# Kernel optimization log

Hardware: AMD Instinct MI355X
Metric: run time of the kernel (lower is better)

## Reference

```python
import jax, jax.numpy as jnp
import numpy as np

B, S, E, H = 4, 2048, 1024, 16
D = E // H


def setup_inputs() -> dict:
    key = jax.random.key(0)
    ks = jax.random.split(key, 6)
    scale = 1.0 / np.sqrt(E).astype(np.float32)
    return {
        "x": jax.random.normal(ks[0], (B, S, E), jnp.float32),
        # positive entries -> cumsum normalizer is well conditioned
        "weight": jax.random.uniform(ks[1], (H, S), jnp.float32, 0.05, 1.0),
        "bias": jax.random.normal(ks[2], (H, S), jnp.float32) * 0.02,
        "inp_w": jax.random.normal(ks[3], (E, E), jnp.float32) * scale,
        "inp_b": jax.random.normal(ks[4], (E,), jnp.float32) * 0.02,
        "out_w": jax.random.normal(ks[5], (E, E), jnp.float32) * scale,
    }


def reference(x, weight, bias, inp_w, inp_b, out_w):
    Bx, Sx, Ex = x.shape
    Hx = weight.shape[0]
    Dx = Ex // Hx
    # input projection (torch Linear: x @ W.T + b)
    x = x @ inp_w.T + inp_b
    # (B,S,E) -> (B,E,S) -> (B,H,D,S)
    xh = x.transpose(0, 2, 1).reshape(Bx, Hx, Dx, Sx)
    # Toeplitz causal matrix per head: M[h,i,j] = weight[h, j-i] if j>=i else 0
    idx = jnp.arange(Sx)
    off = idx[None, :] - idx[:, None]  # (S,S)
    M = jnp.where(off >= 0, weight[:, off], jnp.zeros((), x.dtype))  # (H,S,S)
    # batched matmul over the sequence axis: y[b,h,d,t] = sum_s x[b,h,d,s] M[h,s,t]
    y = jnp.einsum('bhds,hst->bhdt', xh, M)
    # cumulative-sum normalization (do_toep_mean=True)
    norm = jnp.cumsum(weight, axis=-1)  # (H,S)
    y = y / norm[None, :, None, :]
    # per-head, per-position bias
    y = y + bias[None, :, None, :]
    # (B,H,D,S) -> (B,E,S) -> (B,S,E)
    y = y.reshape(Bx, Ex, Sx).transpose(0, 2, 1)
    # output projection (no bias)
    return y @ out_w.T
```

## Files before the change

kernel.cpp:

```cpp
#include <hip/hip_runtime.h>

typedef unsigned short u16;
typedef __attribute__((ext_vector_type(4))) float f32x4;
typedef __attribute__((ext_vector_type(8))) __bf16 bf16x8;

__device__ __forceinline__ u16 f2bf(float f) {
  unsigned u = __builtin_bit_cast(unsigned, f);
  u = u + 0x7fffu + ((u >> 16) & 1u);
  return (u16)(u >> 16);
}

__device__ __forceinline__ void load_lds16(const void* g, void* l) {
  __builtin_amdgcn_global_load_lds((__attribute__((address_space(1))) void*)g,
                                   (__attribute__((address_space(3))) void*)l,
                                   16, 0, 0);
}

__device__ __forceinline__ f32x4 MF(bf16x8 a, bf16x8 b, f32x4 c) {
  return __builtin_amdgcn_mfma_f32_16x16x32_bf16(a, b, c, 0, 0, 0);
}

__global__ __launch_bounds__(256) void prep_all(const float* __restrict__ x,
                                                const float* __restrict__ inp_w,
                                                const float* __restrict__ out_w,
                                                const float* __restrict__ weight,
                                                u16* __restrict__ Xb,
                                                u16* __restrict__ Wb,
                                                u16* __restrict__ OWb,
                                                float* __restrict__ normB,
                                                u16* __restrict__ V) {
  const int bx = blockIdx.x, tid = threadIdx.x;
  if (bx < 10240) {
    const float* src; u16* dst; int i;
    if (bx < 8192)      { src = x;     dst = Xb;  i = bx * 256 + tid; }
    else if (bx < 9216) { src = inp_w; dst = Wb;  i = (bx - 8192) * 256 + tid; }
    else                { src = out_w; dst = OWb; i = (bx - 9216) * 256 + tid; }
    const float4 v = ((const float4*)src)[i];
    ushort4 o;
    o.x = f2bf(v.x); o.y = f2bf(v.y); o.z = f2bf(v.z); o.w = f2bf(v.w);
    ((ushort4*)dst)[i] = o;
    return;
  }
  if (bx < 10256) {
    const int h = bx - 10240;
    __shared__ float ts[256];
    float v[8];
    const float* src = weight + h * 2048 + tid * 8;
    float s = 0.f;
#pragma unroll
    for (int j = 0; j < 8; ++j) v[j] = src[j];
#pragma unroll
    for (int j = 0; j < 8; ++j) { s += v[j]; v[j] = s; }
    ts[tid] = s;
    __syncthreads();
    float xx = s;
#pragma unroll
    for (int d = 1; d < 256; d <<= 1) {
      float y = (tid >= d) ? ts[tid - d] : 0.f;
      __syncthreads();
      xx += y;
      ts[tid] = xx;
      __syncthreads();
    }
    const float excl = xx - s;
    float* dst = normB + h * 2048 + tid * 8;
#pragma unroll
    for (int j = 0; j < 8; ++j) dst[j] = excl + v[j];
    return;
  }
  {
    const int bb = bx - 10256;
    const int h = bb & 15, tb = bb >> 4;
    __shared__ u16 wl[2048];
#pragma unroll
    for (int j = 0; j < 8; ++j) wl[tid * 8 + j] = f2bf(weight[h * 2048 + tid * 8 + j]);
    __syncthreads();
#pragma unroll
    for (int i = 0; i < 8; ++i) {
      const int cid = i * 256 + tid;
      const int row = cid >> 4, c = cid & 15;
      const int t = tb * 128 + row;
      const int j0 = c * 8;
      unsigned v[8];
#pragma unroll
      for (int jj = 0; jj < 8; ++jj) {
        const int j = j0 + jj;
        v[jj] = (t >= j) ? (unsigned)wl[t - j] : 0u;
      }
      uint4 o;
      o.x = v[0] | (v[1] << 16); o.y = v[2] | (v[3] << 16);
      o.z = v[4] | (v[5] << 16); o.w = v[6] | (v[7] << 16);
      *(uint4*)(V + ((size_t)(h * 2048 + t)) * 128 + j0) = o;
    }
  }
}

template <bool BIAS, bool F32OUT, int DEC>
__global__ __launch_bounds__(256) void gemm_nt4(const u16* __restrict__ A,
                                                const u16* __restrict__ B,
                                                void* __restrict__ C,
                                                const float* __restrict__ bias,
                                                int K, int lda, int ldb, int ldc) {
  __shared__ __align__(16) u16 As[2][128 * 64];
  __shared__ __align__(16) u16 Bs[2][128 * 64];
  const int tid = threadIdx.x;
  const int lane = tid & 63, wv = tid >> 6;
  const int wm = wv >> 1, wn = wv & 1;
  const int l15 = lane & 15, g = lane >> 4;

  const int flat = (int)blockIdx.x;
  int m0, n0;
  if (DEC == 0) {
    const int xcd = flat & 7, i = flat >> 3;
    m0 = (i & 7) * 128;
    n0 = ((xcd << 3) + (i >> 3)) * 128;
  } else {
    const int sw = (flat & 7) * 64 + (flat >> 3);
    m0 = (sw >> 3) * 128;
    n0 = (sw & 7) * 128;
  }

  const int NT = K >> 6;

  auto stage = [&](int t, int bi) {
    const int kt = t << 6;
#pragma unroll
    for (int i = 0; i < 4; ++i) {
      const int c = i * 256 + tid;
      const int row = c >> 3, cc = c & 7;
      load_lds16(A + (size_t)(m0 + row) * lda + kt + ((cc ^ (row & 7)) << 3),
                 &As[bi][i * 2048 + wv * 512]);
    }
#pragma unroll
    for (int i = 0; i < 4; ++i) {
      const int c = i * 256 + tid;
      const int row = c >> 3, cc = c & 7;
      load_lds16(B + (size_t)(n0 + row) * ldb + kt + ((cc ^ (row & 7)) << 3),
                 &Bs[bi][i * 2048 + wv * 512]);
    }
  };

  f32x4 acc[4][4] = {};
  stage(0, 0);
  __syncthreads();
  int cur = 0;
  for (int t = 0; t < NT; ++t) {
    if (t + 1 < NT) stage(t + 1, cur ^ 1);
#pragma unroll
    for (int kh = 0; kh < 2; ++kh) {
      bf16x8 af[4], bf[4];
#pragma unroll
      for (int mf = 0; mf < 4; ++mf) {
        const int row = wm * 64 + mf * 16 + l15;
        af[mf] = *(const bf16x8*)(&As[cur][row * 64 + ((((kh << 2) + g) ^ (row & 7)) << 3)]);
      }
#pragma unroll
      for (int nf = 0; nf < 4; ++nf) {
        const int row = wn * 64 + nf * 16 + l15;
        bf[nf] = *(const bf16x8*)(&Bs[cur][row * 64 + ((((kh << 2) + g) ^ (row & 7)) << 3)]);
      }
      __builtin_amdgcn_s_setprio(1);
#pragma unroll
      for (int mf = 0; mf < 4; ++mf)
#pragma unroll
        for (int nf = 0; nf < 4; ++nf)
          acc[mf][nf] = MF(af[mf], bf[nf], acc[mf][nf]);
      __builtin_amdgcn_s_setprio(0);
    }
    __syncthreads();
    cur ^= 1;
  }

#pragma unroll
  for (int mf = 0; mf < 4; ++mf) {
#pragma unroll
    for (int r = 0; r < 4; ++r) {
      const int row = m0 + wm * 64 + mf * 16 + g * 4 + r;
      const float bb = BIAS ? bias[row] : 0.f;
#pragma unroll
      for (int nf = 0; nf < 4; ++nf) {
        const int col = n0 + wn * 64 + nf * 16 + l15;
        const float v = acc[mf][nf][r] + bb;
        if (F32OUT)
          ((float*)C)[(size_t)row * ldc + col] = v;
        else
          ((u16*)C)[(size_t)row * ldc + col] = f2bf(v);
      }
    }
  }
}

__global__ __launch_bounds__(256) void toep_conv(const u16* __restrict__ X1t,
                                                 const u16* __restrict__ V,
                                                 const float* __restrict__ normB,
                                                 const float* __restrict__ biasB,
                                                 u16* __restrict__ Y2b) {
  __shared__ __align__(16) u16 As[3][128 * 64];
  __shared__ __align__(16) u16 Xs[3][64 * 64];
  const int tid = threadIdx.x;
  const int lane = tid & 63, wv = tid >> 6;
  const int l15 = lane & 15, g = lane >> 4;

  const int x = (int)blockIdx.x;
  const int h = (x & 7) + 8 * ((x >> 3) & 1);
  const int pb = x >> 4;
  const int pair = pb & 7, b = pb >> 3;

  const u16* Vh = V + (size_t)h * 2048 * 128;
  const u16* Xrow = X1t + (size_t)h * 64 * 8192 + b * 2048;

#pragma unroll 1
  for (int ti = 0; ti < 2; ++ti) {
    const int tt = ti ? pair : 15 - pair;
    const int t0 = tt * 128;
    const int Q = (tt + 1) * 2;
    f32x4 acc[2][4] = {};

    auto stage = [&](int q, int bufi) {
      const int st = q >> 1, k = q & 1;
      const int s0 = st * 128 + k * 64;
#pragma unroll
      for (int i = 0; i < 2; ++i) {
        const int c = i * 256 + tid;
        const int row = c >> 3, cc = c & 7;
        load_lds16(Xrow + (size_t)row * 8192 + s0 + ((cc ^ (row & 7)) * 8),
                   &Xs[bufi][i * 2048 + wv * 512]);
      }
      const u16* Ab = Vh + (size_t)(tt - st) * 128 * 128 + k * 64;
#pragma unroll
      for (int i = 0; i < 4; ++i) {
        const int c = i * 256 + tid;
        const int row = c >> 3, cc = c & 7;
        load_lds16(Ab + row * 128 + ((cc ^ (row & 7)) * 8),
                   &As[bufi][i * 2048 + wv * 512]);
      }
    };

    stage(0, 0);
    if (Q > 1) stage(1, 1);
    asm volatile("s_waitcnt vmcnt(6)" ::: "memory");
    __builtin_amdgcn_sched_barrier(0);
    __builtin_amdgcn_s_barrier();
    asm volatile("" ::: "memory");

    int cur = 0;
    for (int q = 0; q < Q; ++q) {
      if (q + 2 < Q) stage(q + 2, (q + 2) % 3);
#pragma unroll
      for (int ks = 0; ks < 2; ++ks) {
        bf16x8 af[2];
#pragma unroll
        for (int tf = 0; tf < 2; ++tf) {
          const int row = wv * 32 + tf * 16 + l15;
          af[tf] = *(const bf16x8*)(&As[cur][row * 64 + (((ks * 4 + g) ^ (row & 7)) * 8)]);
        }
        __builtin_amdgcn_s_setprio(1);
#pragma unroll
        for (int nf = 0; nf < 4; ++nf) {
          const int row = nf * 16 + l15;
          const bf16x8 bv = *(const bf16x8*)(&Xs[cur][row * 64 + (((ks * 4 + g) ^ (row & 7)) * 8)]);
#pragma unroll
          for (int tf = 0; tf < 2; ++tf)
            acc[tf][nf] = MF(af[tf], bv, acc[tf][nf]);
        }
        __builtin_amdgcn_s_setprio(0);
      }
      if (q + 2 < Q)      asm volatile("s_waitcnt vmcnt(6)" ::: "memory");
      else if (q + 1 < Q) asm volatile("s_waitcnt vmcnt(0)" ::: "memory");
      __builtin_amdgcn_sched_barrier(0);
      __builtin_amdgcn_s_barrier();
      asm volatile("" ::: "memory");
      cur = (cur == 2) ? 0 : cur + 1;
    }

#pragma unroll
    for (int tf = 0; tf < 2; ++tf) {
#pragma unroll
      for (int r = 0; r < 4; ++r) {
        const int t = t0 + wv * 32 + tf * 16 + g * 4 + r;
        const float inv = 1.0f / normB[h * 2048 + t];
        const float bb = biasB[h * 2048 + t];
#pragma unroll
        for (int nf = 0; nf < 4; ++nf) {
          const int d = nf * 16 + l15;
          Y2b[(size_t)(b * 2048 + t) * 1024 + h * 64 + d] = f2bf(acc[tf][nf][r] * inv + bb);
        }
      }
    }
  }
}

extern "C" void kernel_launch(void* const* d_in, const int* in_sizes, int n_in,
                              void* d_out, int out_size, void* d_ws, size_t ws_size,
                              hipStream_t stream) {
  (void)in_sizes; (void)n_in; (void)out_size; (void)ws_size;
  const float* x      = (const float*)d_in[0];
  const float* weight = (const float*)d_in[1];
  const float* biasB  = (const float*)d_in[2];
  const float* inp_w  = (const float*)d_in[3];
  const float* inp_b  = (const float*)d_in[4];
  const float* out_w  = (const float*)d_in[5];

  char* ws = (char*)d_ws;
  u16* Xb    = (u16*)(ws + 0);
  u16* X1t   = (u16*)(ws + (size_t)(16u << 20));
  u16* Y2b   = (u16*)(ws + (size_t)(32u << 20));
  u16* Wb    = (u16*)(ws + (size_t)(48u << 20));
  u16* OWb   = (u16*)(ws + (size_t)(50u << 20));
  float* normB = (float*)(ws + (size_t)(53u << 20));
  u16* Vt    = (u16*)(ws + (size_t)(56u << 20));

  prep_all<<<10512, 256, 0, stream>>>(x, inp_w, out_w, weight, Xb, Wb, OWb, normB, Vt);

  gemm_nt4<true, false, 0><<<512, 256, 0, stream>>>(
      Wb, Xb, (void*)X1t, inp_b, 1024, 1024, 1024, 8192);

  toep_conv<<<512, 256, 0, stream>>>(X1t, Vt, normB, biasB, Y2b);

  gemm_nt4<false, true, 1><<<512, 256, 0, stream>>>(
      Y2b, OWb, d_out, nullptr, 1024, 1024, 1024, 1024);
}
```

Measured before the change: 98.03 us.

## Overlap out-proj weight cast and Toeplitz prep with the input-projection GEMM

Splits the prep kernel so only the x and inp_w casts run before the first GEMM. The out_w cast, cumsum normalizer and Toeplitz V construction become extra blocks appended to the first GEMM launch. The aim is to hide that prep work behind GEMM execution and trim the serial prep kernel. In exchange, the prep blocks inherit the GEMM kernel's LDS footprint and launch configuration, which may reduce occupancy.

```diff
diff --git a/kernel.cpp b/kernel.cpp
--- a/kernel.cpp
+++ b/kernel.cpp
@@ -20,29 +20,36 @@
   return __builtin_amdgcn_mfma_f32_16x16x32_bf16(a, b, c, 0, 0, 0);
 }
 
-__global__ __launch_bounds__(256) void prep_all(const float* __restrict__ x,
+__global__ __launch_bounds__(256) void prep_pre(const float* __restrict__ x,
                                                 const float* __restrict__ inp_w,
-                                                const float* __restrict__ out_w,
-                                                const float* __restrict__ weight,
                                                 u16* __restrict__ Xb,
-                                                u16* __restrict__ Wb,
-                                                u16* __restrict__ OWb,
-                                                float* __restrict__ normB,
-                                                u16* __restrict__ V) {
+                                                u16* __restrict__ Wb) {
   const int bx = blockIdx.x, tid = threadIdx.x;
-  if (bx < 10240) {
-    const float* src; u16* dst; int i;
-    if (bx < 8192)      { src = x;     dst = Xb;  i = bx * 256 + tid; }
-    else if (bx < 9216) { src = inp_w; dst = Wb;  i = (bx - 8192) * 256 + tid; }
-    else                { src = out_w; dst = OWb; i = (bx - 9216) * 256 + tid; }
-    const float4 v = ((const float4*)src)[i];
+  const float* src; u16* dst; int i;
+  if (bx < 8192) { src = x;     dst = Xb; i = bx * 256 + tid; }
+  else           { src = inp_w; dst = Wb; i = (bx - 8192) * 256 + tid; }
+  const float4 v = ((const float4*)src)[i];
+  ushort4 o;
+  o.x = f2bf(v.x); o.y = f2bf(v.y); o.z = f2bf(v.z); o.w = f2bf(v.w);
+  ((ushort4*)dst)[i] = o;
+}
+
+__device__ void prep_post_block(int ex, int tid,
+                                const float* __restrict__ out_w,
+                                const float* __restrict__ weight,
+                                u16* __restrict__ OWb,
+                                float* __restrict__ normB,
+                                u16* __restrict__ V) {
+  if (ex < 1024) {
+    const int i = ex * 256 + tid;
+    const float4 v = ((const float4*)out_w)[i];
     ushort4 o;
     o.x = f2bf(v.x); o.y = f2bf(v.y); o.z = f2bf(v.z); o.w = f2bf(v.w);
-    ((ushort4*)dst)[i] = o;
+    ((ushort4*)OWb)[i] = o;
     return;
   }
-  if (bx < 10256) {
-    const int h = bx - 10240;
+  if (ex < 1040) {
+    const int h = ex - 1024;
     __shared__ float ts[256];
     float v[8];
     const float* src = weight + h * 2048 + tid * 8;
@@ -69,7 +76,7 @@
     return;
   }
   {
-    const int bb = bx - 10256;
+    const int bb = ex - 1040;
     const int h = bb & 15, tb = bb >> 4;
     __shared__ u16 wl[2048];
 #pragma unroll
@@ -95,12 +102,22 @@
   }
 }
 
-template <bool BIAS, bool F32OUT, int DEC>
+template <bool BIAS, bool F32OUT, int DEC, bool POST>
 __global__ __launch_bounds__(256) void gemm_nt4(const u16* __restrict__ A,
                                                 const u16* __restrict__ B,
                                                 void* __restrict__ C,
                                                 const float* __restrict__ bias,
-                                                int K, int lda, int ldb, int ldc) {
+                                                int K, int lda, int ldb, int ldc,
+                                                const float* __restrict__ out_w,
+                                                const float* __restrict__ weight,
+                                                u16* __restrict__ OWb,
+                                                float* __restrict__ normB,
+                                                u16* __restrict__ Vt) {
+  const int flatAll = (int)blockIdx.x;
+  if (POST && flatAll >= 512) {
+    prep_post_block(flatAll - 512, threadIdx.x, out_w, weight, OWb, normB, Vt);
+    return;
+  }
   __shared__ __align__(16) u16 As[2][128 * 64];
   __shared__ __align__(16) u16 Bs[2][128 * 64];
   const int tid = threadIdx.x;
@@ -108,7 +125,7 @@
   const int wm = wv >> 1, wn = wv & 1;
   const int l15 = lane & 15, g = lane >> 4;
 
-  const int flat = (int)blockIdx.x;
+  const int flat = flatAll;
   int m0, n0;
   if (DEC == 0) {
     const int xcd = flat & 7, i = flat >> 3;
@@ -310,13 +327,15 @@
   float* normB = (float*)(ws + (size_t)(53u << 20));
   u16* Vt    = (u16*)(ws + (size_t)(56u << 20));
 
-  prep_all<<<10512, 256, 0, stream>>>(x, inp_w, out_w, weight, Xb, Wb, OWb, normB, Vt);
-
-  gemm_nt4<true, false, 0><<<512, 256, 0, stream>>>(
-      Wb, Xb, (void*)X1t, inp_b, 1024, 1024, 1024, 8192);
+  prep_pre<<<9216, 256, 0, stream>>>(x, inp_w, Xb, Wb);
+
+  gemm_nt4<true, false, 0, true><<<1808, 256, 0, stream>>>(
+      Wb, Xb, (void*)X1t, inp_b, 1024, 1024, 1024, 8192,
+      out_w, weight, OWb, normB, Vt);
 
   toep_conv<<<512, 256, 0, stream>>>(X1t, Vt, normB, biasB, Y2b);
 
-  gemm_nt4<false, true, 1><<<512, 256, 0, stream>>>(
-      Y2b, OWb, d_out, nullptr, 1024, 1024, 1024, 1024);
-}
+  gemm_nt4<false, true, 1, false><<<512, 256, 0, stream>>>(
+      Y2b, OWb, d_out, nullptr, 1024, 1024, 1024, 1024,
+      nullptr, nullptr, nullptr, nullptr, nullptr);
+}
```

Result: no change. 96.20 us (median of 3 runs) (-1.9%).
